# Kernel tuning notes

Hardware: AMD Instinct MI355X
Metric: run time of the kernel (lower is better)

## Reference

```python
import jax, jax.numpy as jnp
import numpy as np

BS, N, F, R, OUT = 8, 512, 512, 16, 512
ALPHA = 0.2

def setup_inputs() -> dict:
    key = jax.random.key(0)
    ks = jax.random.split(key, 16)
    w = lambda k, shp: (jax.random.normal(k, shp, dtype=jnp.float32) * 0.05)
    return {
        'x_ori': jax.random.normal(ks[0], (BS, N, F), dtype=jnp.float32),
        'x': jax.random.normal(ks[1], (BS, N, F), dtype=jnp.float32),
        'c': jax.random.normal(ks[2], (BS, 1, F), dtype=jnp.float32),
        'adj': jax.random.randint(ks[3], (BS, N, N, R), 0, 2, dtype=jnp.int32),
        'Wfc': w(ks[4], (F, F)),
        'Wdc': w(ks[5], (F, F)),
        'Wqv': w(ks[6], (2 * F, F)),
        'Wkv': w(ks[7], (2 * F, F)),
        'Wqc': w(ks[8], (F, F)),
        'Wkc': w(ks[9], (F, F)),
        'Wa': w(ks[10], (2 * F, R)),
        'Wu': w(ks[11], (2 * F, OUT)),
    }

def reference(x_ori, x, c, adj, Wfc, Wdc, Wqv, Wkv, Wqc, Wkc, Wa, Wu):
    # relation-context modulation vector m: [bs,1,F]
    m = jnp.matmul(jax.nn.elu(jnp.matmul(c, Wfc)), Wdc)
    nodes = jnp.concatenate([x, x_ori], axis=2)          # [bs,N,2F]
    xq = jnp.matmul(nodes, Wqv) * jnp.matmul(m, Wqc)     # [bs,N,F]
    xk = jnp.matmul(nodes, Wkv) * jnp.matmul(m, Wkc)     # [bs,N,F]
    # scores[b,i,j,r] = leakyrelu(xq_i . Wa[:F,r] + xk_j . Wa[F:,r])
    # (equivalent to cat([xq_i,xk_j]) @ Wa without materializing [bs,N,N,2F])
    sq = jnp.matmul(xq, Wa[:F])                          # [bs,N,R]
    sk = jnp.matmul(xk, Wa[F:])                          # [bs,N,R]
    scores = jax.nn.leaky_relu(sq[:, :, None, :] + sk[:, None, :, :], ALPHA)
    adj_f = adj.astype(scores.dtype)                     # [bs,N,N,R]
    s = jnp.sum(scores * adj_f, axis=3)                  # [bs,N,N]
    mask = jnp.sum(adj_f, axis=3) > 0
    attn = jax.nn.softmax(jnp.where(mask, s, jnp.float32(-9e15)), axis=2)
    new_x = jnp.matmul(attn, x)                          # [bs,N,F]
    return jnp.matmul(jnp.concatenate([x, new_x], axis=2), Wu)
```

## Files before the change

kernel.cpp:

```cpp
#include <hip/hip_runtime.h>
#include <hip/hip_bf16.h>
#include <cstddef>
#include <cstdint>

static constexpr int BSZ  = 8;
static constexpr int NN   = 512;
static constexpr int FF   = 512;
static constexpr int RR   = 16;
static constexpr int TWOF = 1024;

typedef __attribute__((ext_vector_type(8))) short short8;
typedef __attribute__((ext_vector_type(4))) float f32x4;

__device__ __forceinline__ ushort bf16_bits(float v) {
    union { __hip_bfloat16 h; ushort u; } cvt;
    cvt.h = __float2bfloat16(v);
    return cvt.u;
}

static constexpr size_t OFF_TB     = 0;
static constexpr size_t OFF_MB     = 16384;
static constexpr size_t OFF_MQ     = 32768;
static constexpr size_t OFF_MK     = 49152;
static constexpr size_t OFF_SQ     = 65536;
static constexpr size_t OFF_SK     = 327680;
static constexpr size_t OFF_WQET   = 589824;
static constexpr size_t OFF_WKET   = 851968;
static constexpr size_t OFF_XBF    = 5308416;
static constexpr size_t OFF_XTBF   = 9502720;
static constexpr size_t OFF_XORIBF = 13697024;
static constexpr size_t OFF_NEWXBF = 17891328;
static constexpr size_t OFF_WUT    = 22085632;

__global__ __launch_bounds__(256) void k_prep(
    const float* __restrict__ x_ori, const float* __restrict__ x,
    const float* __restrict__ c, const float* __restrict__ Wfc,
    const float* __restrict__ Wu,
    ushort* __restrict__ xori_bf, ushort* __restrict__ x_bf,
    ushort* __restrict__ xT_bf, ushort* __restrict__ WuT,
    float* __restrict__ tb)
{
    int blk = blockIdx.x;
    int t = threadIdx.x;
    if (blk < 1024) {
        int idx = blk * 256 + t;
        float4 a = ((const float4*)x_ori)[idx * 2];
        float4 b = ((const float4*)x_ori)[idx * 2 + 1];
        uint4 s;
        s.x = (uint)bf16_bits(a.x) | ((uint)bf16_bits(a.y) << 16);
        s.y = (uint)bf16_bits(a.z) | ((uint)bf16_bits(a.w) << 16);
        s.z = (uint)bf16_bits(b.x) | ((uint)bf16_bits(b.y) << 16);
        s.w = (uint)bf16_bits(b.z) | ((uint)bf16_bits(b.w) << 16);
        ((uint4*)xori_bf)[idx] = s;
    } else if (blk < 3072) {
        __shared__ float tile[32][33];
        int bb = blk - 1024;
        int f0 = (bb & 15) * 32, i0 = ((bb >> 4) & 15) * 32, b = bb >> 8;
        int cc = t & 31, r0 = t >> 5;
#pragma unroll
        for (int rr = 0; rr < 32; rr += 8) {
            int i = i0 + r0 + rr;
            float v = x[((size_t)b * NN + i) * FF + f0 + cc];
            tile[r0 + rr][cc] = v;
            x_bf[((size_t)b * NN + i) * FF + f0 + cc] = bf16_bits(v);
        }
        __syncthreads();
#pragma unroll
        for (int rr = 0; rr < 32; rr += 8) {
            int f = f0 + r0 + rr;
            xT_bf[((size_t)b * FF + f) * NN + i0 + cc] = bf16_bits(tile[cc][r0 + rr]);
        }
    } else if (blk < 3584) {
        __shared__ float tile2[32][33];
        int bb = blk - 3072;
        int f0 = (bb & 31) * 32, o0 = (bb >> 5) * 32;
        int cc = t & 31, r0 = t >> 5;
#pragma unroll
        for (int rr = 0; rr < 32; rr += 8)
            tile2[r0 + rr][cc] = Wu[(size_t)(f0 + r0 + rr) * FF + o0 + cc];
        __syncthreads();
#pragma unroll
        for (int rr = 0; rr < 32; rr += 8)
            WuT[(size_t)(o0 + r0 + rr) * TWOF + f0 + cc] = bf16_bits(tile2[cc][r0 + rr]);
    } else {
        __shared__ float red1[8][32];
        int bb = blk - 3584;
        int b = bb >> 4, f0 = (bb & 15) * 32;
        int f = t & 31, kq = t >> 5;
        const float* vb = c + (size_t)b * FF;
        float acc = 0.f;
        int ks = kq * 64;
#pragma unroll 8
        for (int k = ks; k < ks + 64; ++k)
            acc = fmaf(vb[k], Wfc[(size_t)k * FF + f0 + f], acc);
        red1[kq][f] = acc;
        __syncthreads();
        if (kq == 0) {
            acc += red1[1][f] + red1[2][f] + red1[3][f] + red1[4][f] +
                   red1[5][f] + red1[6][f] + red1[7][f];
            tb[(size_t)b * FF + f0 + f] = (acc > 0.f) ? acc : expm1f(acc);
        }
    }
}

__global__ __launch_bounds__(256) void k_matvec(const float* __restrict__ vin,
                                                const float* __restrict__ W,
                                                float* __restrict__ vout) {
    __shared__ float red[8][32];
    int b = blockIdx.y;
    int f0 = blockIdx.x * 32;
    int t = threadIdx.x;
    int f = t & 31, kq = t >> 5;
    const float* vb = vin + (size_t)b * FF;
    float acc = 0.f;
    int ks = kq * 64;
#pragma unroll 8
    for (int k = ks; k < ks + 64; ++k)
        acc = fmaf(vb[k], W[(size_t)k * FF + f0 + f], acc);
    red[kq][f] = acc;
    __syncthreads();
    if (kq == 0) {
        acc += red[1][f] + red[2][f] + red[3][f] + red[4][f] +
               red[5][f] + red[6][f] + red[7][f];
        vout[(size_t)b * FF + f0 + f] = acc;
    }
}

__global__ __launch_bounds__(256) void k_mqk(const float* __restrict__ m,
                                             const float* __restrict__ Wqc,
                                             const float* __restrict__ Wkc,
                                             float* __restrict__ mq,
                                             float* __restrict__ mk) {
    __shared__ float redq[8][32];
    __shared__ float redk[8][32];
    int b = blockIdx.y;
    int f0 = blockIdx.x * 32;
    int t = threadIdx.x;
    int f = t & 31, kq = t >> 5;
    const float* mb = m + (size_t)b * FF;
    float aq = 0.f, ak = 0.f;
    int ks = kq * 64;
#pragma unroll 8
    for (int k = ks; k < ks + 64; ++k) {
        float mv = mb[k];
        aq = fmaf(mv, Wqc[(size_t)k * FF + f0 + f], aq);
        ak = fmaf(mv, Wkc[(size_t)k * FF + f0 + f], ak);
    }
    redq[kq][f] = aq;
    redk[kq][f] = ak;
    __syncthreads();
    if (kq == 0) {
        aq += redq[1][f] + redq[2][f] + redq[3][f] + redq[4][f] +
              redq[5][f] + redq[6][f] + redq[7][f];
        ak += redk[1][f] + redk[2][f] + redk[3][f] + redk[4][f] +
              redk[5][f] + redk[6][f] + redk[7][f];
        mq[(size_t)b * FF + f0 + f] = aq;
        mk[(size_t)b * FF + f0 + f] = ak;
    }
}

__global__ __launch_bounds__(256) void k_weff(const float* __restrict__ Wqv,
                                              const float* __restrict__ Wkv,
                                              const float* __restrict__ Wa,
                                              const float* __restrict__ mqv,
                                              const float* __restrict__ mkv,
                                              ushort* __restrict__ WqEt,
                                              ushort* __restrict__ WkEt) {
    int z = blockIdx.z;
    const float* W = z ? Wkv : Wqv;
    const float* mvec = z ? mkv : mqv;
    ushort* WeffT = z ? WkEt : WqEt;
    int waRowOff = z ? FF : 0;

    __shared__ float4 wa4[FF * 4];
    int tid = threadIdx.x;
    int b = blockIdx.y;
    const float* mv = mvec + (size_t)b * FF;
#pragma unroll
    for (int qq = 0; qq < 8; ++qq) {
        int idx = tid + qq * 256;
        int f = idx >> 2, rq = idx & 3;
        float4 w = *reinterpret_cast<const float4*>(Wa + (size_t)(waRowOff + f) * RR + rq * 4);
        float s = mv[f];
        float4 o;
        o.x = w.x * s; o.y = w.y * s; o.z = w.z * s; o.w = w.w * s;
        wa4[idx] = o;
    }
    __syncthreads();
    int k_l = tid >> 2, r4 = tid & 3;
    int k = blockIdx.x * 64 + k_l;
    const float4* Wrow4 = reinterpret_cast<const float4*>(W + (size_t)k * FF);
    float4 acc = {0.f, 0.f, 0.f, 0.f};
#pragma unroll 4
    for (int f4 = 0; f4 < FF / 4; ++f4) {
        float4 w = Wrow4[f4];
        float4 v0 = wa4[(f4 * 4 + 0) * 4 + r4];
        float4 v1 = wa4[(f4 * 4 + 1) * 4 + r4];
        float4 v2 = wa4[(f4 * 4 + 2) * 4 + r4];
        float4 v3 = wa4[(f4 * 4 + 3) * 4 + r4];
        acc.x = fmaf(w.x, v0.x, acc.x); acc.y = fmaf(w.x, v0.y, acc.y);
        acc.z = fmaf(w.x, v0.z, acc.z); acc.w = fmaf(w.x, v0.w, acc.w);
        acc.x = fmaf(w.y, v1.x, acc.x); acc.y = fmaf(w.y, v1.y, acc.y);
        acc.z = fmaf(w.y, v1.z, acc.z); acc.w = fmaf(w.y, v1.w, acc.w);
        acc.x = fmaf(w.z, v2.x, acc.x); acc.y = fmaf(w.z, v2.y, acc.y);
        acc.z = fmaf(w.z, v2.z, acc.z); acc.w = fmaf(w.z, v2.w, acc.w);
        acc.x = fmaf(w.w, v3.x, acc.x); acc.y = fmaf(w.w, v3.y, acc.y);
        acc.z = fmaf(w.w, v3.z, acc.z); acc.w = fmaf(w.w, v3.w, acc.w);
    }
    WeffT[((size_t)b * RR + r4 * 4 + 0) * TWOF + k] = bf16_bits(acc.x);
    WeffT[((size_t)b * RR + r4 * 4 + 1) * TWOF + k] = bf16_bits(acc.y);
    WeffT[((size_t)b * RR + r4 * 4 + 2) * TWOF + k] = bf16_bits(acc.z);
    WeffT[((size_t)b * RR + r4 * 4 + 3) * TWOF + k] = bf16_bits(acc.w);
}

__global__ __launch_bounds__(256) void k_sqsk(const ushort* __restrict__ x_bf,
                                              const ushort* __restrict__ xori_bf,
                                              const ushort* __restrict__ WqEt,
                                              const ushort* __restrict__ WkEt,
                                              float* __restrict__ sq,
                                              float* __restrict__ sk) {
    int t = threadIdx.x;
    int b = blockIdx.y;
    int m0 = blockIdx.x * 32;
    int lane = t & 63, w = t >> 6;
    int sub = w & 1, isK = w >> 1;
    int m_l = lane & 15, q = lane >> 4;
    int row = m0 + sub * 16 + m_l;
    const ushort* Bt = (isK ? WkEt : WqEt) + ((size_t)b * RR + m_l) * TWOF;
    f32x4 acc = {0.f, 0.f, 0.f, 0.f};
#pragma unroll
    for (int k0 = 0; k0 < TWOF; k0 += 32) {
        const ushort* src = (k0 < FF) ? x_bf : xori_bf;
        int kc = k0 & (FF - 1);
        short8 af = *(const short8*)(src + ((size_t)b * NN + row) * FF + kc + q * 8);
        short8 bf = *(const short8*)(Bt + k0 + q * 8);
        acc = __builtin_amdgcn_mfma_f32_16x16x32_bf16(af, bf, acc, 0, 0, 0);
    }
    float* dst = isK ? sk : sq;
#pragma unroll
    for (int r = 0; r < 4; ++r) {
        int i = m0 + sub * 16 + q * 4 + r;
        dst[((size_t)b * NN + i) * RR + m_l] = acc[r];
    }
}

__global__ __launch_bounds__(256) void k_attn_pv(const int* __restrict__ adj,
                                                 const float* __restrict__ sq,
                                                 const float* __restrict__ sk,
                                                 const ushort* __restrict__ xT_bf,
                                                 ushort* __restrict__ newx_bf) {
    constexpr int ZS = 520;
    __shared__ float  zbuf[16 * ZS];
    __shared__ ushort P[16 * ZS];
    __shared__ float  rowsum[16];
    int t = threadIdx.x;
    int b = blockIdx.y;
    int m0 = blockIdx.x * 16;

    {
        int r = t >> 4, cc = t & 15;
        int i = m0 + r;
        const float4* sqp = (const float4*)(sq + ((size_t)b * NN + i) * RR);
        float4 q0 = sqp[0], q1 = sqp[1], q2 = sqp[2], q3 = sqp[3];
        float sv[16] = {q0.x, q0.y, q0.z, q0.w, q1.x, q1.y, q1.z, q1.w,
                        q2.x, q2.y, q2.z, q2.w, q3.x, q3.y, q3.z, q3.w};
#pragma unroll 4
        for (int it = 0; it < 32; ++it) {
            int j = it * 16 + cc;
            size_t base = (((size_t)b * NN + i) * NN + j) * RR;
            const int4* ap = (const int4*)(adj + base);
            int4 a0 = ap[0], a1 = ap[1], a2 = ap[2], a3 = ap[3];
            const float4* kp = (const float4*)(sk + ((size_t)b * NN + j) * RR);
            float4 s0 = kp[0], s1 = kp[1], s2 = kp[2], s3 = kp[3];
            int sum_adj = a0.x + a0.y + a0.z + a0.w + a1.x + a1.y + a1.z + a1.w +
                          a2.x + a2.y + a2.z + a2.w + a3.x + a3.y + a3.z + a3.w;
            float ssum = 0.f;
#define LR_TERM(SVAL, AVAL, RIDX)                                   \
            { float v_ = sv[RIDX] + (SVAL);                         \
              v_ = fmaxf(v_, 0.2f * v_);                            \
              ssum = fmaf(v_, (float)(AVAL), ssum); }
            LR_TERM(s0.x, a0.x, 0)  LR_TERM(s0.y, a0.y, 1)
            LR_TERM(s0.z, a0.z, 2)  LR_TERM(s0.w, a0.w, 3)
            LR_TERM(s1.x, a1.x, 4)  LR_TERM(s1.y, a1.y, 5)
            LR_TERM(s1.z, a1.z, 6)  LR_TERM(s1.w, a1.w, 7)
            LR_TERM(s2.x, a2.x, 8)  LR_TERM(s2.y, a2.y, 9)
            LR_TERM(s2.z, a2.z, 10) LR_TERM(s2.w, a2.w, 11)
            LR_TERM(s3.x, a3.x, 12) LR_TERM(s3.y, a3.y, 13)
            LR_TERM(s3.z, a3.z, 14) LR_TERM(s3.w, a3.w, 15)
#undef LR_TERM
            zbuf[r * ZS + j] = (sum_adj > 0) ? ssum : -9e15f;
        }
    }
    __syncthreads();

    {
        int w = t >> 6, lane = t & 63;
        int rr = w * 4 + (lane >> 4);
        int cc = lane & 15;
        const float* zr = &zbuf[rr * ZS];
        float mx = -3.0e38f;
#pragma unroll 8
        for (int it = 0; it < 32; ++it) mx = fmaxf(mx, zr[it * 16 + cc]);
#pragma unroll
        for (int off = 1; off < 16; off <<= 1) mx = fmaxf(mx, __shfl_xor(mx, off, 64));
        float sum = 0.f;
        ushort* pr = &P[rr * ZS];
#pragma unroll 8
        for (int it = 0; it < 32; ++it) {
            float e = __expf(zr[it * 16 + cc] - mx);
            pr[it * 16 + cc] = bf16_bits(e);
            sum += e;
        }
#pragma unroll
        for (int off = 1; off < 16; off <<= 1) sum += __shfl_xor(sum, off, 64);
        if (cc == 0) rowsum[rr] = sum;
    }
    __syncthreads();

    {
        int w = t >> 6, lane = t & 63;
        int m_l = lane & 15, q = lane >> 4;
        int n0w = w * 128;
        f32x4 acc[8] = {};
        const ushort* xTb = xT_bf + (size_t)b * FF * NN;
        for (int k0 = 0; k0 < NN; k0 += 32) {
            short8 af = *(const short8*)(&P[m_l * ZS + k0 + q * 8]);
#pragma unroll
            for (int nb = 0; nb < 8; ++nb) {
                int n = n0w + nb * 16 + m_l;
                short8 bfr = *(const short8*)(xTb + (size_t)n * NN + k0 + q * 8);
                acc[nb] = __builtin_amdgcn_mfma_f32_16x16x32_bf16(af, bfr, acc[nb], 0, 0, 0);
            }
        }
        float inv[4];
#pragma unroll
        for (int rg = 0; rg < 4; ++rg) inv[rg] = 1.f / rowsum[q * 4 + rg];
#pragma unroll
        for (int nb = 0; nb < 8; ++nb) {
#pragma unroll
            for (int rg = 0; rg < 4; ++rg) {
                int i = m0 + q * 4 + rg;
                int f = n0w + nb * 16 + m_l;
                newx_bf[((size_t)b * NN + i) * FF + f] = bf16_bits(acc[nb][rg] * inv[rg]);
            }
        }
    }
}

__global__ __launch_bounds__(256) void k_gemm(const ushort* __restrict__ A1, size_t sA1,
                                              const ushort* __restrict__ A2, size_t sA2,
                                              const ushort* __restrict__ BT, size_t sBT,
                                              float* __restrict__ Cf, size_t sC,
                                              int K, int ldBT) {
    __shared__ ushort As[2][64 * 40];
    __shared__ ushort Bs[2][64 * 40];
    int t = threadIdx.x;
    int n0 = blockIdx.x * 64, m0 = blockIdx.y * 64, b = blockIdx.z;
    int row = t >> 2, c8 = (t & 3) * 8;
    int lane = t & 63, w = t >> 6;
    int m_l = lane & 15, q = lane >> 4;
    f32x4 acc[4] = {{0.f,0.f,0.f,0.f},{0.f,0.f,0.f,0.f},{0.f,0.f,0.f,0.f},{0.f,0.f,0.f,0.f}};
    const ushort* BTb = BT + (size_t)b * sBT;
    for (int k0 = 0; k0 < K; k0 += 64) {
#pragma unroll
        for (int h = 0; h < 2; ++h) {
            int kk = k0 + h * 32;
            const ushort* Aab; int kc;
            if (kk < FF) { Aab = A1 + (size_t)b * sA1; kc = kk; }
            else         { Aab = A2 + (size_t)b * sA2; kc = kk - FF; }
            uint4 av = *(const uint4*)(Aab + (size_t)(m0 + row) * FF + kc + c8);
            uint4 bv = *(const uint4*)(BTb + (size_t)(n0 + row) * ldBT + kk + c8);
            *(uint4*)(&As[h][row * 40 + c8]) = av;
            *(uint4*)(&Bs[h][row * 40 + c8]) = bv;
        }
        __syncthreads();
#pragma unroll
        for (int h = 0; h < 2; ++h) {
            short8 af = *(const short8*)(&As[h][(w * 16 + m_l) * 40 + q * 8]);
#pragma unroll
            for (int nb = 0; nb < 4; ++nb) {
                short8 bfr = *(const short8*)(&Bs[h][(nb * 16 + m_l) * 40 + q * 8]);
                acc[nb] = __builtin_amdgcn_mfma_f32_16x16x32_bf16(af, bfr, acc[nb], 0, 0, 0);
            }
        }
        __syncthreads();
    }
#pragma unroll
    for (int nb = 0; nb < 4; ++nb) {
#pragma unroll
        for (int r = 0; r < 4; ++r) {
            int mi = m0 + w * 16 + q * 4 + r;
            int ni = n0 + nb * 16 + m_l;
            Cf[(size_t)b * sC + (size_t)mi * FF + ni] = acc[nb][r];
        }
    }
}

extern "C" void kernel_launch(void* const* d_in, const int* in_sizes, int n_in,
                              void* d_out, int out_size, void* d_ws, size_t ws_size,
                              hipStream_t stream) {
    const float* x_ori = (const float*)d_in[0];
    const float* x     = (const float*)d_in[1];
    const float* c     = (const float*)d_in[2];
    const int*   adj   = (const int*)d_in[3];
    const float* Wfc   = (const float*)d_in[4];
    const float* Wdc   = (const float*)d_in[5];
    const float* Wqv   = (const float*)d_in[6];
    const float* Wkv   = (const float*)d_in[7];
    const float* Wqc   = (const float*)d_in[8];
    const float* Wkc   = (const float*)d_in[9];
    const float* Wa    = (const float*)d_in[10];
    const float* Wu    = (const float*)d_in[11];
    float* out = (float*)d_out;

    char* ws = (char*)d_ws;
    float*  tb      = (float*)(ws + OFF_TB);
    float*  mb      = (float*)(ws + OFF_MB);
    float*  mq      = (float*)(ws + OFF_MQ);
    float*  mk      = (float*)(ws + OFF_MK);
    float*  sq      = (float*)(ws + OFF_SQ);
    float*  sk      = (float*)(ws + OFF_SK);
    ushort* WqEt    = (ushort*)(ws + OFF_WQET);
    ushort* WkEt    = (ushort*)(ws + OFF_WKET);
    ushort* x_bf    = (ushort*)(ws + OFF_XBF);
    ushort* xT_bf   = (ushort*)(ws + OFF_XTBF);
    ushort* xori_bf = (ushort*)(ws + OFF_XORIBF);
    ushort* newx_bf = (ushort*)(ws + OFF_NEWXBF);
    ushort* WuT     = (ushort*)(ws + OFF_WUT);

    dim3 blk(256);

    k_prep<<<dim3(3712), blk, 0, stream>>>(x_ori, x, c, Wfc, Wu,
                                           xori_bf, x_bf, xT_bf, WuT, tb);

    k_matvec<<<dim3(16, BSZ), blk, 0, stream>>>(tb, Wdc, mb);
    k_mqk<<<dim3(16, BSZ), blk, 0, stream>>>(mb, Wqc, Wkc, mq, mk);

    k_weff<<<dim3(16, BSZ, 2), blk, 0, stream>>>(Wqv, Wkv, Wa, mq, mk, WqEt, WkEt);

    k_sqsk<<<dim3(16, BSZ), blk, 0, stream>>>(x_bf, xori_bf, WqEt, WkEt, sq, sk);

    k_attn_pv<<<dim3(32, BSZ), blk, 0, stream>>>(adj, sq, sk, xT_bf, newx_bf);

    k_gemm<<<dim3(8, 8, BSZ), blk, 0, stream>>>(
        x_bf, (size_t)NN * FF, newx_bf, (size_t)NN * FF,
        WuT, (size_t)0, out, (size_t)NN * FF, TWOF, TWOF);
}
```

Baseline: 302.9 us.

## Fuse new_x @ Wu_bottom into attention kernel, split output GEMM into x half

Splits the final output GEMM into two parts. The x @ Wu[:F] half runs early as a separate K=512 GEMM writing to out. The new_x @ Wu[F:] half is fused into the attention kernel: new_x is kept in shared memory as bf16 and multiplied by WuT columns, and the result is added to out. This removes the new_x global round trip and one kernel stage. The attention kernel now uses 512 threads and more shared memory, and each block reads all of WuT's second half, with no LDS staging, for only 16 rows, which can increase global/L2 traffic.

```diff
diff --git a/kernel.cpp b/kernel.cpp
--- a/kernel.cpp
+++ b/kernel.cpp
@@ -29,7 +29,6 @@
 static constexpr size_t OFF_XBF    = 5308416;
 static constexpr size_t OFF_XTBF   = 9502720;
 static constexpr size_t OFF_XORIBF = 13697024;
-static constexpr size_t OFF_NEWXBF = 17891328;
 static constexpr size_t OFF_WUT    = 22085632;
 
 __global__ __launch_bounds__(256) void k_prep(
@@ -244,29 +243,76 @@
     }
 }
 
-__global__ __launch_bounds__(256) void k_attn_pv(const int* __restrict__ adj,
+__global__ __launch_bounds__(256) void k_gemm(const ushort* __restrict__ A1,
+                                              const ushort* __restrict__ BT,
+                                              float* __restrict__ Cf,
+                                              int ldBT) {
+    __shared__ ushort As[2][64 * 40];
+    __shared__ ushort Bs[2][64 * 40];
+    int t = threadIdx.x;
+    int n0 = blockIdx.x * 64, m0 = blockIdx.y * 64, b = blockIdx.z;
+    int row = t >> 2, c8 = (t & 3) * 8;
+    int lane = t & 63, w = t >> 6;
+    int m_l = lane & 15, q = lane >> 4;
+    f32x4 acc[4] = {{0.f,0.f,0.f,0.f},{0.f,0.f,0.f,0.f},{0.f,0.f,0.f,0.f},{0.f,0.f,0.f,0.f}};
+    const ushort* Ab = A1 + (size_t)b * NN * FF;
+    for (int k0 = 0; k0 < FF; k0 += 64) {
+#pragma unroll
+        for (int h = 0; h < 2; ++h) {
+            int kk = k0 + h * 32;
+            uint4 av = *(const uint4*)(Ab + (size_t)(m0 + row) * FF + kk + c8);
+            uint4 bv = *(const uint4*)(BT + (size_t)(n0 + row) * ldBT + kk + c8);
+            *(uint4*)(&As[h][row * 40 + c8]) = av;
+            *(uint4*)(&Bs[h][row * 40 + c8]) = bv;
+        }
+        __syncthreads();
+#pragma unroll
+        for (int h = 0; h < 2; ++h) {
+            short8 af = *(const short8*)(&As[h][(w * 16 + m_l) * 40 + q * 8]);
+#pragma unroll
+            for (int nb = 0; nb < 4; ++nb) {
+                short8 bfr = *(const short8*)(&Bs[h][(nb * 16 + m_l) * 40 + q * 8]);
+                acc[nb] = __builtin_amdgcn_mfma_f32_16x16x32_bf16(af, bfr, acc[nb], 0, 0, 0);
+            }
+        }
+        __syncthreads();
+    }
+#pragma unroll
+    for (int nb = 0; nb < 4; ++nb) {
+#pragma unroll
+        for (int r = 0; r < 4; ++r) {
+            int mi = m0 + w * 16 + q * 4 + r;
+            int ni = n0 + nb * 16 + m_l;
+            Cf[((size_t)b * NN + mi) * FF + ni] = acc[nb][r];
+        }
+    }
+}
+
+__global__ __launch_bounds__(512) void k_attn_pv(const int* __restrict__ adj,
                                                  const float* __restrict__ sq,
                                                  const float* __restrict__ sk,
                                                  const ushort* __restrict__ xT_bf,
-                                                 ushort* __restrict__ newx_bf) {
+                                                 const ushort* __restrict__ WuT,
+                                                 float* __restrict__ out) {
     constexpr int ZS = 520;
     __shared__ float  zbuf[16 * ZS];
     __shared__ ushort P[16 * ZS];
+    __shared__ ushort NX[16 * ZS];
     __shared__ float  rowsum[16];
     int t = threadIdx.x;
     int b = blockIdx.y;
     int m0 = blockIdx.x * 16;
 
     {
-        int r = t >> 4, cc = t & 15;
+        int r = t >> 5, cc = t & 31;
         int i = m0 + r;
         const float4* sqp = (const float4*)(sq + ((size_t)b * NN + i) * RR);
         float4 q0 = sqp[0], q1 = sqp[1], q2 = sqp[2], q3 = sqp[3];
         float sv[16] = {q0.x, q0.y, q0.z, q0.w, q1.x, q1.y, q1.z, q1.w,
                         q2.x, q2.y, q2.z, q2.w, q3.x, q3.y, q3.z, q3.w};
 #pragma unroll 4
-        for (int it = 0; it < 32; ++it) {
-            int j = it * 16 + cc;
+        for (int it = 0; it < 16; ++it) {
+            int j = it * 32 + cc;
             size_t base = (((size_t)b * NN + i) * NN + j) * RR;
             const int4* ap = (const int4*)(adj + base);
             int4 a0 = ap[0], a1 = ap[1], a2 = ap[2], a3 = ap[3];
@@ -294,25 +340,23 @@
     __syncthreads();
 
     {
-        int w = t >> 6, lane = t & 63;
-        int rr = w * 4 + (lane >> 4);
-        int cc = lane & 15;
+        int rr = t >> 5, cc = t & 31;
         const float* zr = &zbuf[rr * ZS];
         float mx = -3.0e38f;
-#pragma unroll 8
-        for (int it = 0; it < 32; ++it) mx = fmaxf(mx, zr[it * 16 + cc]);
-#pragma unroll
-        for (int off = 1; off < 16; off <<= 1) mx = fmaxf(mx, __shfl_xor(mx, off, 64));
+#pragma unroll 4
+        for (int it = 0; it < 16; ++it) mx = fmaxf(mx, zr[it * 32 + cc]);
+#pragma unroll
+        for (int off = 1; off < 32; off <<= 1) mx = fmaxf(mx, __shfl_xor(mx, off, 32));
         float sum = 0.f;
         ushort* pr = &P[rr * ZS];
-#pragma unroll 8
-        for (int it = 0; it < 32; ++it) {
-            float e = __expf(zr[it * 16 + cc] - mx);
-            pr[it * 16 + cc] = bf16_bits(e);
+#pragma unroll 4
+        for (int it = 0; it < 16; ++it) {
+            float e = __expf(zr[it * 32 + cc] - mx);
+            pr[it * 32 + cc] = bf16_bits(e);
             sum += e;
         }
 #pragma unroll
-        for (int off = 1; off < 16; off <<= 1) sum += __shfl_xor(sum, off, 64);
+        for (int off = 1; off < 32; off <<= 1) sum += __shfl_xor(sum, off, 32);
         if (cc == 0) rowsum[rr] = sum;
     }
     __syncthreads();
@@ -320,13 +364,13 @@
     {
         int w = t >> 6, lane = t & 63;
         int m_l = lane & 15, q = lane >> 4;
-        int n0w = w * 128;
-        f32x4 acc[8] = {};
+        int n0w = w * 64;
+        f32x4 acc[4] = {};
         const ushort* xTb = xT_bf + (size_t)b * FF * NN;
         for (int k0 = 0; k0 < NN; k0 += 32) {
             short8 af = *(const short8*)(&P[m_l * ZS + k0 + q * 8]);
 #pragma unroll
-            for (int nb = 0; nb < 8; ++nb) {
+            for (int nb = 0; nb < 4; ++nb) {
                 int n = n0w + nb * 16 + m_l;
                 short8 bfr = *(const short8*)(xTb + (size_t)n * NN + k0 + q * 8);
                 acc[nb] = __builtin_amdgcn_mfma_f32_16x16x32_bf16(af, bfr, acc[nb], 0, 0, 0);
@@ -336,62 +380,38 @@
 #pragma unroll
         for (int rg = 0; rg < 4; ++rg) inv[rg] = 1.f / rowsum[q * 4 + rg];
 #pragma unroll
-        for (int nb = 0; nb < 8; ++nb) {
+        for (int nb = 0; nb < 4; ++nb) {
+#pragma unroll
+            for (int rg = 0; rg < 4; ++rg) {
+                NX[(q * 4 + rg) * ZS + n0w + nb * 16 + m_l] = bf16_bits(acc[nb][rg] * inv[rg]);
+            }
+        }
+    }
+    __syncthreads();
+
+    {
+        int w = t >> 6, lane = t & 63;
+        int m_l = lane & 15, q = lane >> 4;
+        int n0w = w * 64;
+        f32x4 acc[4] = {};
+        for (int k0 = 0; k0 < FF; k0 += 32) {
+            short8 af = *(const short8*)(&NX[m_l * ZS + k0 + q * 8]);
+#pragma unroll
+            for (int nb = 0; nb < 4; ++nb) {
+                int o = n0w + nb * 16 + m_l;
+                short8 bfr = *(const short8*)(WuT + (size_t)o * TWOF + FF + k0 + q * 8);
+                acc[nb] = __builtin_amdgcn_mfma_f32_16x16x32_bf16(af, bfr, acc[nb], 0, 0, 0);
+            }
+        }
+#pragma unroll
+        for (int nb = 0; nb < 4; ++nb) {
 #pragma unroll
             for (int rg = 0; rg < 4; ++rg) {
                 int i = m0 + q * 4 + rg;
-                int f = n0w + nb * 16 + m_l;
-                newx_bf[((size_t)b * NN + i) * FF + f] = bf16_bits(acc[nb][rg] * inv[rg]);
+                int o = n0w + nb * 16 + m_l;
+                size_t idx = ((size_t)b * NN + i) * FF + o;
+                out[idx] = out[idx] + acc[nb][rg];
             }
-        }
-    }
-}
-
-__global__ __launch_bounds__(256) void k_gemm(const ushort* __restrict__ A1, size_t sA1,
-                                              const ushort* __restrict__ A2, size_t sA2,
-                                              const ushort* __restrict__ BT, size_t sBT,
-                                              float* __restrict__ Cf, size_t sC,
-                                              int K, int ldBT) {
-    __shared__ ushort As[2][64 * 40];
-    __shared__ ushort Bs[2][64 * 40];
-    int t = threadIdx.x;
-    int n0 = blockIdx.x * 64, m0 = blockIdx.y * 64, b = blockIdx.z;
-    int row = t >> 2, c8 = (t & 3) * 8;
-    int lane = t & 63, w = t >> 6;
-    int m_l = lane & 15, q = lane >> 4;
-    f32x4 acc[4] = {{0.f,0.f,0.f,0.f},{0.f,0.f,0.f,0.f},{0.f,0.f,0.f,0.f},{0.f,0.f,0.f,0.f}};
-    const ushort* BTb = BT + (size_t)b * sBT;
-    for (int k0 = 0; k0 < K; k0 += 64) {
-#pragma unroll
-        for (int h = 0; h < 2; ++h) {
-            int kk = k0 + h * 32;
-            const ushort* Aab; int kc;
-            if (kk < FF) { Aab = A1 + (size_t)b * sA1; kc = kk; }
-            else         { Aab = A2 + (size_t)b * sA2; kc = kk - FF; }
-            uint4 av = *(const uint4*)(Aab + (size_t)(m0 + row) * FF + kc + c8);
-            uint4 bv = *(const uint4*)(BTb + (size_t)(n0 + row) * ldBT + kk + c8);
-            *(uint4*)(&As[h][row * 40 + c8]) = av;
-            *(uint4*)(&Bs[h][row * 40 + c8]) = bv;
-        }
-        __syncthreads();
-#pragma unroll
-        for (int h = 0; h < 2; ++h) {
-            short8 af = *(const short8*)(&As[h][(w * 16 + m_l) * 40 + q * 8]);
-#pragma unroll
-            for (int nb = 0; nb < 4; ++nb) {
-                short8 bfr = *(const short8*)(&Bs[h][(nb * 16 + m_l) * 40 + q * 8]);
-                acc[nb] = __builtin_amdgcn_mfma_f32_16x16x32_bf16(af, bfr, acc[nb], 0, 0, 0);
-            }
-        }
-        __syncthreads();
-    }
-#pragma unroll
-    for (int nb = 0; nb < 4; ++nb) {
-#pragma unroll
-        for (int r = 0; r < 4; ++r) {
-            int mi = m0 + w * 16 + q * 4 + r;
-            int ni = n0 + nb * 16 + m_l;
-            Cf[(size_t)b * sC + (size_t)mi * FF + ni] = acc[nb][r];
         }
     }
 }
@@ -425,7 +445,6 @@
     ushort* x_bf    = (ushort*)(ws + OFF_XBF);
     ushort* xT_bf   = (ushort*)(ws + OFF_XTBF);
     ushort* xori_bf = (ushort*)(ws + OFF_XORIBF);
-    ushort* newx_bf = (ushort*)(ws + OFF_NEWXBF);
     ushort* WuT     = (ushort*)(ws + OFF_WUT);
 
     dim3 blk(256);
@@ -433,6 +452,8 @@
     k_prep<<<dim3(3712), blk, 0, stream>>>(x_ori, x, c, Wfc, Wu,
                                            xori_bf, x_bf, xT_bf, WuT, tb);
 
+    k_gemm<<<dim3(8, 8, BSZ), blk, 0, stream>>>(x_bf, WuT, out, TWOF);
+
     k_matvec<<<dim3(16, BSZ), blk, 0, stream>>>(tb, Wdc, mb);
     k_mqk<<<dim3(16, BSZ), blk, 0, stream>>>(mb, Wqc, Wkc, mq, mk);
 
@@ -440,9 +461,5 @@
 
     k_sqsk<<<dim3(16, BSZ), blk, 0, stream>>>(x_bf, xori_bf, WqEt, WkEt, sq, sk);
 
-    k_attn_pv<<<dim3(32, BSZ), blk, 0, stream>>>(adj, sq, sk, xT_bf, newx_bf);
-
-    k_gemm<<<dim3(8, 8, BSZ), blk, 0, stream>>>(
-        x_bf, (size_t)NN * FF, newx_bf, (size_t)NN * FF,
-        WuT, (size_t)0, out, (size_t)NN * FF, TWOF, TWOF);
-}
+    k_attn_pv<<<dim3(32, BSZ), dim3(512), 0, stream>>>(adj, sq, sk, xT_bf, WuT, out);
+}
```

Measured after the change: 307.4 us. No clear change (+1.5%).
